# Performance work log

Hardware: AMD Instinct MI355X
Metric: run time of the kernel (lower is better)

## Reference

```python
import jax, jax.numpy as jnp
import numpy as np

B, S, E = 2, 2048, 2048
NH, NKV = 32, 8
HD = E // NH  # 64


def apply_rope(x, cos, sin):
    # x: [B, S, H, D]; cos/sin: [S, D]
    s, d = x.shape[1], x.shape[3]
    c = cos[:s, :d][None, :, None, :]
    sn = sin[:s, :d][None, :, None, :]
    x_rot = jnp.concatenate([-x[..., d // 2:], x[..., : d // 2]], axis=-1)
    return x * c + x_rot * sn


def setup_inputs() -> dict:
    key = jax.random.key(0)
    ks = jax.random.split(key, 6)
    x = jax.random.normal(ks[0], (B, S, E), dtype=jnp.float32)
    mask = jnp.ones((B, S), dtype=bool)
    # RoPE tables [S, HD]
    inv_freq = 1.0 / (10000.0 ** (jnp.arange(0, HD, 2, dtype=jnp.float32) / HD))
    freqs = jnp.arange(S, dtype=jnp.float32)[:, None] * inv_freq[None, :]
    emb = jnp.concatenate([freqs, freqs], axis=-1)  # [S, HD]
    cos = jnp.cos(emb)
    sin = jnp.sin(emb)
    sc = 1.0 / np.sqrt(E)
    Wq = jax.random.normal(ks[1], (E, E), dtype=jnp.float32) * sc
    Wk = jax.random.normal(ks[2], (NKV * HD, E), dtype=jnp.float32) * sc
    Wv = jax.random.normal(ks[3], (NKV * HD, E), dtype=jnp.float32) * sc
    Wo = jax.random.normal(ks[4], (E, E), dtype=jnp.float32) * sc
    return {"x": x, "mask": mask, "cos": cos, "sin": sin,
            "Wq": Wq, "Wk": Wk, "Wv": Wv, "Wo": Wo}


def reference(x, mask, cos, sin, Wq, Wk, Wv, Wo):
    b, s, e = x.shape
    scale = 1.0 / np.sqrt(HD)
    q = (x @ Wq.T).reshape(b, s, NH, HD)
    k = (x @ Wk.T).reshape(b, s, NKV, HD)
    v = (x @ Wv.T).reshape(b, s, NKV, HD)
    q = apply_rope(q, cos, sin)
    k = apply_rope(k, cos, sin)
    rep = NH // NKV
    # expand kv heads: [B,S,NKV,HD] -> [B,S,NH,HD]
    k = jnp.repeat(k, rep, axis=2)
    v = jnp.repeat(v, rep, axis=2)
    # [B,H,S,S]
    scores = jnp.einsum('bqhd,bkhd->bhqk', q, k) * scale
    causal = jnp.tril(jnp.ones((s, s), dtype=bool))
    combined = mask[:, None, None, :] & causal[None, None, :, :]
    scores = jnp.where(combined, scores, -jnp.inf)
    attn = jax.nn.softmax(scores, axis=-1)
    ctx = jnp.einsum('bhqk,bkhd->bqhd', attn, v).reshape(b, s, e)
    return ctx @ Wo.T
```

## Files before the change

kernel.cpp:

```cpp
#include <hip/hip_runtime.h>


typedef __attribute__((ext_vector_type(4))) float f32x4;
typedef __attribute__((ext_vector_type(16))) float f32x16;
typedef __attribute__((ext_vector_type(8))) __bf16 bf16x8;

__device__ __forceinline__ short f2bf(float f) {
  union { float f; unsigned u; } c; c.f = f;
  unsigned r = c.u + 0x7FFFu + ((c.u >> 16) & 1u);
  return (short)(r >> 16);
}

#define GLOAD16(g, l)                                                      \
  __builtin_amdgcn_global_load_lds(                                        \
      (const __attribute__((address_space(1))) unsigned int*)(g),          \
      (__attribute__((address_space(3))) unsigned int*)(l), 16, 0, 0)

__device__ __forceinline__ f32x4 mfma16(bf16x8 a, bf16x8 b, f32x4 c) {
  return __builtin_amdgcn_mfma_f32_16x16x32_bf16(a, b, c, 0, 0, 0);
}
__device__ __forceinline__ f32x16 mfma32(bf16x8 a, bf16x8 b, f32x16 c) {
  return __builtin_amdgcn_mfma_f32_32x32x16_bf16(a, b, c, 0, 0, 0);
}

__global__ void conv_bf16(const float* __restrict__ src, short* __restrict__ dst, int n) {
  int i = (blockIdx.x * blockDim.x + threadIdx.x) * 4;
  if (i >= n) return;
  float4 v = *(const float4*)(src + i);
  *(short4*)(dst + i) = make_short4(f2bf(v.x), f2bf(v.y), f2bf(v.z), f2bf(v.w));
}

__global__ __launch_bounds__(256, 2)
void gemm_bt(const short* __restrict__ A, const short* __restrict__ B,
             float* __restrict__ C, int M, int N, int K) {
  __shared__ short As[2][128 * 32];
  __shared__ short Bs[2][128 * 32];
  const int tid = threadIdx.x;
  const int lane = tid & 63;
  const int wm = (tid >> 6) >> 1;
  const int wn = (tid >> 6) & 1;
  const int m0 = blockIdx.x * 128;
  const int n0 = blockIdx.y * 128;
  const int kr = lane >> 4;
  const int lc = lane & 15;

  f32x4 acc[4][4] = {};

  const int lin0 = tid * 16;
  const int row0 = lin0 >> 6;
  const int slot0 = (lin0 >> 4) & 3;
  const int gs0 = slot0 ^ ((row0 >> 1) & 3);
  const int row1 = row0 + 64;
  const int gs1 = slot0 ^ ((row1 >> 1) & 3);
  const short* Ag0 = A + (size_t)(m0 + row0) * K + gs0 * 8;
  const short* Ag1 = A + (size_t)(m0 + row1) * K + gs1 * 8;
  const short* Bg0 = B + (size_t)(n0 + row0) * K + gs0 * 8;
  const short* Bg1 = B + (size_t)(n0 + row1) * K + gs1 * 8;
  const int dA0 = tid * 8;
  const int dA1 = tid * 8 + 2048;

  auto STAGE = [&](int k0, int buf) {
    GLOAD16(Ag0 + k0, &As[buf][dA0]);
    GLOAD16(Ag1 + k0, &As[buf][dA1]);
    GLOAD16(Bg0 + k0, &Bs[buf][dA0]);
    GLOAD16(Bg1 + k0, &Bs[buf][dA1]);
  };

  STAGE(0, 0);
  __syncthreads();
  int cur = 0;
  for (int k0 = 0; k0 < K; k0 += 32) {
    if (k0 + 32 < K) STAGE(k0 + 32, cur ^ 1);
    bf16x8 af[4], bfr[4];
#pragma unroll
    for (int i = 0; i < 4; ++i) {
      int r = wm * 64 + i * 16 + lc;
      af[i] = *(const bf16x8*)(&As[cur][r * 32 + ((kr ^ ((r >> 1) & 3)) << 3)]);
    }
#pragma unroll
    for (int j = 0; j < 4; ++j) {
      int r = wn * 64 + j * 16 + lc;
      bfr[j] = *(const bf16x8*)(&Bs[cur][r * 32 + ((kr ^ ((r >> 1) & 3)) << 3)]);
    }
#pragma unroll
    for (int i = 0; i < 4; ++i)
#pragma unroll
      for (int j = 0; j < 4; ++j)
        acc[i][j] = mfma16(af[i], bfr[j], acc[i][j]);
    __syncthreads();
    cur ^= 1;
  }
#pragma unroll
  for (int i = 0; i < 4; ++i) {
    int r0 = m0 + wm * 64 + i * 16 + kr * 4;
#pragma unroll
    for (int j = 0; j < 4; ++j) {
      int c = n0 + wn * 64 + j * 16 + lc;
#pragma unroll
      for (int ii = 0; ii < 4; ++ii)
        C[(size_t)(r0 + ii) * N + c] = acc[i][j][ii];
    }
  }
}

__global__ void rope_q(const float* __restrict__ qf, const float* __restrict__ cosT,
                       const float* __restrict__ sinT, short* __restrict__ qr) {
  int g = blockIdx.x * blockDim.x + threadIdx.x;
  int row = g >> 10;
  int rem = g & 1023;
  int h = rem >> 5, d = rem & 31;
  int s = row & 2047;
  float c = cosT[s * 64 + d], sn = sinT[s * 64 + d];
  size_t base = (size_t)row * 2048 + h * 64 + d;
  float x0 = qf[base], x1 = qf[base + 32];
  qr[base] = f2bf(x0 * c - x1 * sn);
  qr[base + 32] = f2bf(x1 * c + x0 * sn);
}

__global__ void rope_k(const float* __restrict__ kvf, const float* __restrict__ cosT,
                       const float* __restrict__ sinT, short* __restrict__ kb) {
  int g = blockIdx.x * blockDim.x + threadIdx.x;
  int row = g >> 8;
  int rem = g & 255;
  int h = rem >> 5, d = rem & 31;
  int s = row & 2047;
  float c = cosT[s * 64 + d], sn = sinT[s * 64 + d];
  size_t bi = (size_t)row * 1024 + h * 64 + d;
  size_t bo = (size_t)row * 512 + h * 64 + d;
  float x0 = kvf[bi], x1 = kvf[bi + 32];
  kb[bo] = f2bf(x0 * c - x1 * sn);
  kb[bo + 32] = f2bf(x1 * c + x0 * sn);
}

__global__ void transpose_v(const float* __restrict__ kvf, short* __restrict__ vt) {
  __shared__ float Ls[64 * 65];
  int s0 = blockIdx.x * 64;
  int h = blockIdx.y;
  int b = blockIdx.z;
  int tid = threadIdx.x;
#pragma unroll
  for (int it = 0; it < 16; ++it) {
    int lin = it * 256 + tid;
    int r = lin >> 6, c = lin & 63;
    float v = kvf[(size_t)(b * 2048 + s0 + r) * 1024 + 512 + h * 64 + c];
    Ls[c * 65 + r] = v;
  }
  __syncthreads();
#pragma unroll
  for (int it = 0; it < 16; ++it) {
    int lin = it * 256 + tid;
    int d = lin >> 6, c2 = lin & 63;
    vt[((size_t)((b * 8 + h) * 64 + d)) * 2048 + s0 + c2] = f2bf(Ls[d * 65 + c2]);
  }
}

__global__ __launch_bounds__(256, 2)
void attn(const short* __restrict__ Q, const short* __restrict__ Kk,
          const short* __restrict__ Vt, short* __restrict__ O) {
  const int qb = (int)gridDim.x - 1 - (int)blockIdx.x;
  const int h = blockIdx.y;
  const int b = blockIdx.z;
  const int kvh = h >> 2;
  const int tid = threadIdx.x;
  const int lane = tid & 63;
  const int w = tid >> 6;
  const int l5 = lane >> 5;
  const int lc5 = lane & 31;
  const int q0 = qb * 128;
  const int qrow = q0 + w * 32 + lc5;

  __shared__ short Ks[2][64 * 64];
  __shared__ short Vs[2][64 * 64];

  bf16x8 qreg[4];
  const short* qbase = Q + (size_t)(b * 2048 + qrow) * 2048 + h * 64 + l5 * 8;
#pragma unroll
  for (int s = 0; s < 4; ++s) qreg[s] = *(const bf16x8*)(qbase + s * 16);

  const int srow = tid >> 3;
  const int sslot = tid & 7;
  const short* kb0 = Kk + (size_t)(b * 2048) * 512 + kvh * 64;
  const short* vb0 = Vt + (size_t)((b * 8 + kvh) * 64) * 2048;

  auto STAGE = [&](int kt, int buf) {
#pragma unroll
    for (int it = 0; it < 2; ++it) {
      int row = srow + it * 32;
      int gs = sslot ^ (row & 7);
      GLOAD16(kb0 + (size_t)(kt * 64 + row) * 512 + gs * 8, &Ks[buf][tid * 8 + it * 2048]);
      GLOAD16(vb0 + (size_t)row * 2048 + kt * 64 + gs * 8, &Vs[buf][tid * 8 + it * 2048]);
    }
  };

  f32x16 oa0 = {}, oa1 = {};
  float mrow = -1e30f, lrow = 0.f;

  const int ktmax = (q0 + 127) >> 6;
  STAGE(0, 0);
  __syncthreads();
  int cur = 0;

  for (int kt = 0; kt <= ktmax; ++kt) {
    if (kt < ktmax) STAGE(kt + 1, cur ^ 1);

    f32x16 sa0 = {}, sa1 = {};
    const int rsw = lc5 & 7;
#pragma unroll
    for (int s = 0; s < 4; ++s) {
      int sw = ((2 * s + l5) ^ rsw) << 3;
      bf16x8 k0f = *(const bf16x8*)(&Ks[cur][lc5 * 64 + sw]);
      bf16x8 k1f = *(const bf16x8*)(&Ks[cur][(32 + lc5) * 64 + sw]);
      sa0 = mfma32(k0f, qreg[s], sa0);
      sa1 = mfma32(k1f, qreg[s], sa1);
    }

    const int kbase = kt * 64 + 4 * l5;
    if (kt * 64 + 63 > q0 + w * 32) {
#pragma unroll
      for (int r = 0; r < 16; ++r) {
        int k = kbase + (r & 3) + 8 * (r >> 2);
        if (k > qrow) sa0[r] = -1e30f;
        if (k + 32 > qrow) sa1[r] = -1e30f;
      }
    }

    float mx = -1e30f;
#pragma unroll
    for (int r = 0; r < 16; ++r) mx = fmaxf(mx, fmaxf(sa0[r], sa1[r]));
    mx = fmaxf(mx, __shfl_xor(mx, 32));
    float nm = fmaxf(mrow, mx);
    float resc = __expf((mrow - nm) * 0.125f);
    mrow = nm;
    float psum = 0.f;
#pragma unroll
    for (int r = 0; r < 16; ++r) {
      float p0 = __expf((sa0[r] - nm) * 0.125f);
      float p1 = __expf((sa1[r] - nm) * 0.125f);
      sa0[r] = p0; sa1[r] = p1;
      psum += p0 + p1;
    }
    psum += __shfl_xor(psum, 32);
    lrow = lrow * resc + psum;
#pragma unroll
    for (int r = 0; r < 16; ++r) { oa0[r] *= resc; oa1[r] *= resc; }

    unsigned pk0[8], pk1[8];
#pragma unroll
    for (int a = 0; a < 8; ++a) {
      asm("v_cvt_pk_bf16_f32 %0, %1, %2" : "=v"(pk0[a]) : "v"(sa0[2 * a]), "v"(sa0[2 * a + 1]));
      asm("v_cvt_pk_bf16_f32 %0, %1, %2" : "=v"(pk1[a]) : "v"(sa1[2 * a]), "v"(sa1[2 * a + 1]));
    }

#pragma unroll
    for (int s = 0; s < 4; ++s) {
      const int c = s & 1;
      unsigned x0 = (s < 2) ? pk0[4 * c + 0] : pk1[4 * c + 0];
      unsigned y0 = (s < 2) ? pk0[4 * c + 2] : pk1[4 * c + 2];
      unsigned x1 = (s < 2) ? pk0[4 * c + 1] : pk1[4 * c + 1];
      unsigned y1 = (s < 2) ? pk0[4 * c + 3] : pk1[4 * c + 3];
      asm("v_permlane32_swap_b32 %0, %1" : "+v"(x0), "+v"(y0));
      asm("v_permlane32_swap_b32 %0, %1" : "+v"(x1), "+v"(y1));
      union { unsigned u[4]; bf16x8 v; } pf;
      pf.u[0] = x0; pf.u[1] = x1; pf.u[2] = y0; pf.u[3] = y1;
      int sw = ((2 * s + l5) ^ rsw) << 3;
      bf16x8 v0 = *(const bf16x8*)(&Vs[cur][lc5 * 64 + sw]);
      bf16x8 v1 = *(const bf16x8*)(&Vs[cur][(32 + lc5) * 64 + sw]);
      oa0 = mfma32(v0, pf.v, oa0);
      oa1 = mfma32(v1, pf.v, oa1);
    }

    __syncthreads();
    cur ^= 1;
  }

  float inv = 1.0f / lrow;
  short* ob = O + (size_t)(b * 2048 + qrow) * 2048 + h * 64 + 4 * l5;
#pragma unroll
  for (int g = 0; g < 4; ++g) {
    *(short4*)(ob + 8 * g) =
        make_short4(f2bf(oa0[4 * g + 0] * inv), f2bf(oa0[4 * g + 1] * inv),
                    f2bf(oa0[4 * g + 2] * inv), f2bf(oa0[4 * g + 3] * inv));
    *(short4*)(ob + 32 + 8 * g) =
        make_short4(f2bf(oa1[4 * g + 0] * inv), f2bf(oa1[4 * g + 1] * inv),
                    f2bf(oa1[4 * g + 2] * inv), f2bf(oa1[4 * g + 3] * inv));
  }
}

extern "C" void kernel_launch(void* const* d_in, const int* in_sizes, int n_in,
                              void* d_out, int out_size, void* d_ws, size_t ws_size,
                              hipStream_t stream) {
  (void)in_sizes; (void)n_in; (void)out_size; (void)ws_size;
  const float* x    = (const float*)d_in[0];
  const float* cosT = (const float*)d_in[2];
  const float* sinT = (const float*)d_in[3];
  const float* Wq   = (const float*)d_in[4];
  const float* Wk   = (const float*)d_in[5];
  const float* Wv   = (const float*)d_in[6];
  const float* Wo   = (const float*)d_in[7];

  char* ws = (char*)d_ws;
  short* xb   = (short*)(ws + 0);
  short* Wqob = (short*)(ws + 16777216);
  short* Wkvb = (short*)(ws + 25165824);
  float* qf   = (float*)(ws + 29360128);
  short* ctx  = (short*)(ws + 29360128);
  float* kvf  = (float*)(ws + 62914560);
  short* qr   = (short*)(ws + 62914560);
  short* kb   = (short*)(ws + 79691776);
  short* vt   = (short*)(ws + 83886080);

  conv_bf16<<<8192, 256, 0, stream>>>(x, xb, 8388608);
  conv_bf16<<<4096, 256, 0, stream>>>(Wq, Wqob, 4194304);
  conv_bf16<<<1024, 256, 0, stream>>>(Wk, Wkvb, 1048576);
  conv_bf16<<<1024, 256, 0, stream>>>(Wv, Wkvb + 1048576, 1048576);

  gemm_bt<<<dim3(32, 16), 256, 0, stream>>>(xb, Wqob, qf, 4096, 2048, 2048);
  gemm_bt<<<dim3(32, 8), 256, 0, stream>>>(xb, Wkvb, kvf, 4096, 1024, 2048);

  rope_k<<<4096, 256, 0, stream>>>(kvf, cosT, sinT, kb);
  transpose_v<<<dim3(32, 8, 2), 256, 0, stream>>>(kvf, vt);
  rope_q<<<16384, 256, 0, stream>>>(qf, cosT, sinT, qr);

  conv_bf16<<<4096, 256, 0, stream>>>(Wo, Wqob, 4194304);

  attn<<<dim3(16, 32, 2), 256, 0, stream>>>(qr, kb, vt, ctx);

  gemm_bt<<<dim3(32, 16), 256, 0, stream>>>(ctx, Wqob, (float*)d_out, 4096, 2048, 2048);
}
```

Baseline: 389.3 us.

## Fuse RoPE and bf16 conversion into projection GEMM epilogues, streamline attention softmax

The Q and KV projection GEMMs now apply RoPE and write bf16 directly in their epilogues. This removes the separate rope_q/rope_k kernels and the fp32 intermediate round-trips, and transpose_v now reads a bf16 V buffer. Q is pre-scaled by scale*log2(e) so attention can use exp2 without the multiply. The rescale of the running max is skipped unless the max grows by more than a threshold. The K/V LDS staging layout also changes to an unswizzled slab layout, and fully masked key tiles skip compute per wave. Risks are possible LDS bank conflicts from the new layout, and accuracy changes from the lazy rescale.

```diff
diff --git a/kernel.cpp b/kernel.cpp
--- a/kernel.cpp
+++ b/kernel.cpp
@@ -4,6 +4,8 @@
 typedef __attribute__((ext_vector_type(4))) float f32x4;
 typedef __attribute__((ext_vector_type(16))) float f32x16;
 typedef __attribute__((ext_vector_type(8))) __bf16 bf16x8;
+
+#define SCL 0.18033688011112042f
 
 __device__ __forceinline__ short f2bf(float f) {
   union { float f; unsigned u; } c; c.f = f;
@@ -30,9 +32,12 @@
   *(short4*)(dst + i) = make_short4(f2bf(v.x), f2bf(v.y), f2bf(v.z), f2bf(v.w));
 }
 
+template <int EPI>
 __global__ __launch_bounds__(256, 2)
 void gemm_bt(const short* __restrict__ A, const short* __restrict__ B,
-             float* __restrict__ C, int M, int N, int K) {
+             float* __restrict__ C, short* __restrict__ outK,
+             short* __restrict__ outV, const float* __restrict__ cosT,
+             const float* __restrict__ sinT, int M, int N, int K) {
   __shared__ short As[2][128 * 32];
   __shared__ short Bs[2][128 * 32];
   const int tid = threadIdx.x;
@@ -90,50 +95,74 @@
     __syncthreads();
     cur ^= 1;
   }
-#pragma unroll
-  for (int i = 0; i < 4; ++i) {
-    int r0 = m0 + wm * 64 + i * 16 + kr * 4;
-#pragma unroll
-    for (int j = 0; j < 4; ++j) {
-      int c = n0 + wn * 64 + j * 16 + lc;
-#pragma unroll
-      for (int ii = 0; ii < 4; ++ii)
-        C[(size_t)(r0 + ii) * N + c] = acc[i][j][ii];
-    }
-  }
-}
-
-__global__ void rope_q(const float* __restrict__ qf, const float* __restrict__ cosT,
-                       const float* __restrict__ sinT, short* __restrict__ qr) {
-  int g = blockIdx.x * blockDim.x + threadIdx.x;
-  int row = g >> 10;
-  int rem = g & 1023;
-  int h = rem >> 5, d = rem & 31;
-  int s = row & 2047;
-  float c = cosT[s * 64 + d], sn = sinT[s * 64 + d];
-  size_t base = (size_t)row * 2048 + h * 64 + d;
-  float x0 = qf[base], x1 = qf[base + 32];
-  qr[base] = f2bf(x0 * c - x1 * sn);
-  qr[base + 32] = f2bf(x1 * c + x0 * sn);
-}
-
-__global__ void rope_k(const float* __restrict__ kvf, const float* __restrict__ cosT,
-                       const float* __restrict__ sinT, short* __restrict__ kb) {
-  int g = blockIdx.x * blockDim.x + threadIdx.x;
-  int row = g >> 8;
-  int rem = g & 255;
-  int h = rem >> 5, d = rem & 31;
-  int s = row & 2047;
-  float c = cosT[s * 64 + d], sn = sinT[s * 64 + d];
-  size_t bi = (size_t)row * 1024 + h * 64 + d;
-  size_t bo = (size_t)row * 512 + h * 64 + d;
-  float x0 = kvf[bi], x1 = kvf[bi + 32];
-  kb[bo] = f2bf(x0 * c - x1 * sn);
-  kb[bo + 32] = f2bf(x1 * c + x0 * sn);
-}
-
-__global__ void transpose_v(const float* __restrict__ kvf, short* __restrict__ vt) {
-  __shared__ float Ls[64 * 65];
+
+  if constexpr (EPI == 0) {
+#pragma unroll
+    for (int i = 0; i < 4; ++i) {
+      int r0 = m0 + wm * 64 + i * 16 + kr * 4;
+#pragma unroll
+      for (int j = 0; j < 4; ++j) {
+        int c = n0 + wn * 64 + j * 16 + lc;
+#pragma unroll
+        for (int ii = 0; ii < 4; ++ii)
+          C[(size_t)(r0 + ii) * N + c] = acc[i][j][ii];
+      }
+    }
+  } else if constexpr (EPI == 1) {
+#pragma unroll
+    for (int i = 0; i < 4; ++i) {
+#pragma unroll
+      for (int ii = 0; ii < 4; ++ii) {
+        int r = m0 + wm * 64 + i * 16 + kr * 4 + ii;
+        int s = r & 2047;
+#pragma unroll
+        for (int jp = 0; jp < 2; ++jp) {
+          int d = jp * 16 + lc;
+          float cs = cosT[s * 64 + d], sn = sinT[s * 64 + d];
+          float x0 = acc[i][jp][ii], x1 = acc[i][jp + 2][ii];
+          size_t base = (size_t)r * N + n0 + wn * 64;
+          outK[base + jp * 16 + lc] = f2bf((x0 * cs - x1 * sn) * SCL);
+          outK[base + (jp + 2) * 16 + lc] = f2bf((x1 * cs + x0 * sn) * SCL);
+        }
+      }
+    }
+  } else {
+    if (n0 < 512) {
+#pragma unroll
+      for (int i = 0; i < 4; ++i) {
+#pragma unroll
+        for (int ii = 0; ii < 4; ++ii) {
+          int r = m0 + wm * 64 + i * 16 + kr * 4 + ii;
+          int s = r & 2047;
+#pragma unroll
+          for (int jp = 0; jp < 2; ++jp) {
+            int d = jp * 16 + lc;
+            float cs = cosT[s * 64 + d], sn = sinT[s * 64 + d];
+            float x0 = acc[i][jp][ii], x1 = acc[i][jp + 2][ii];
+            size_t base = (size_t)r * 512 + n0 + wn * 64;
+            outK[base + jp * 16 + lc] = f2bf(x0 * cs - x1 * sn);
+            outK[base + (jp + 2) * 16 + lc] = f2bf(x1 * cs + x0 * sn);
+          }
+        }
+      }
+    } else {
+#pragma unroll
+      for (int i = 0; i < 4; ++i) {
+#pragma unroll
+        for (int ii = 0; ii < 4; ++ii) {
+          int r = m0 + wm * 64 + i * 16 + kr * 4 + ii;
+#pragma unroll
+          for (int j = 0; j < 4; ++j)
+            outV[(size_t)r * 512 + (n0 - 512) + wn * 64 + j * 16 + lc] =
+                f2bf(acc[i][j][ii]);
+        }
+      }
+    }
+  }
+}
+
+__global__ void transpose_v(const short* __restrict__ vtmp, short* __restrict__ vt) {
+  __shared__ short Ls[64 * 66];
   int s0 = blockIdx.x * 64;
   int h = blockIdx.y;
   int b = blockIdx.z;
@@ -142,15 +171,14 @@
   for (int it = 0; it < 16; ++it) {
     int lin = it * 256 + tid;
     int r = lin >> 6, c = lin & 63;
-    float v = kvf[(size_t)(b * 2048 + s0 + r) * 1024 + 512 + h * 64 + c];
-    Ls[c * 65 + r] = v;
+    Ls[c * 66 + r] = vtmp[(size_t)(b * 2048 + s0 + r) * 512 + h * 64 + c];
   }
   __syncthreads();
 #pragma unroll
   for (int it = 0; it < 16; ++it) {
     int lin = it * 256 + tid;
     int d = lin >> 6, c2 = lin & 63;
-    vt[((size_t)((b * 8 + h) * 64 + d)) * 2048 + s0 + c2] = f2bf(Ls[d * 65 + c2]);
+    vt[((size_t)((b * 8 + h) * 64 + d)) * 2048 + s0 + c2] = Ls[d * 66 + c2];
   }
 }
 
@@ -169,27 +197,22 @@
   const int q0 = qb * 128;
   const int qrow = q0 + w * 32 + lc5;
 
-  __shared__ short Ks[2][64 * 64];
-  __shared__ short Vs[2][64 * 64];
+  __shared__ short Ks[2][4096];
+  __shared__ short Vs[2][4096];
 
   bf16x8 qreg[4];
   const short* qbase = Q + (size_t)(b * 2048 + qrow) * 2048 + h * 64 + l5 * 8;
 #pragma unroll
   for (int s = 0; s < 4; ++s) qreg[s] = *(const bf16x8*)(qbase + s * 16);
 
-  const int srow = tid >> 3;
-  const int sslot = tid & 7;
-  const short* kb0 = Kk + (size_t)(b * 2048) * 512 + kvh * 64;
-  const short* vb0 = Vt + (size_t)((b * 8 + kvh) * 64) * 2048;
+  const short* kbs = Kk + (size_t)b * 2048 * 512 + kvh * 64;
+  const short* vbs = Vt + (size_t)((b * 8 + kvh) * 64) * 2048;
 
   auto STAGE = [&](int kt, int buf) {
-#pragma unroll
-    for (int it = 0; it < 2; ++it) {
-      int row = srow + it * 32;
-      int gs = sslot ^ (row & 7);
-      GLOAD16(kb0 + (size_t)(kt * 64 + row) * 512 + gs * 8, &Ks[buf][tid * 8 + it * 2048]);
-      GLOAD16(vb0 + (size_t)row * 2048 + kt * 64 + gs * 8, &Vs[buf][tid * 8 + it * 2048]);
-    }
+    GLOAD16(kbs + (size_t)(kt * 64 + lane) * 512 + w * 8, &Ks[buf][tid * 8]);
+    GLOAD16(kbs + (size_t)(kt * 64 + lane) * 512 + (w + 4) * 8, &Ks[buf][tid * 8 + 2048]);
+    GLOAD16(vbs + (size_t)lane * 2048 + kt * 64 + w * 8, &Vs[buf][tid * 8]);
+    GLOAD16(vbs + (size_t)lane * 2048 + kt * 64 + (w + 4) * 8, &Vs[buf][tid * 8 + 2048]);
   };
 
   f32x16 oa0 = {}, oa1 = {};
@@ -203,70 +226,70 @@
   for (int kt = 0; kt <= ktmax; ++kt) {
     if (kt < ktmax) STAGE(kt + 1, cur ^ 1);
 
-    f32x16 sa0 = {}, sa1 = {};
-    const int rsw = lc5 & 7;
-#pragma unroll
-    for (int s = 0; s < 4; ++s) {
-      int sw = ((2 * s + l5) ^ rsw) << 3;
-      bf16x8 k0f = *(const bf16x8*)(&Ks[cur][lc5 * 64 + sw]);
-      bf16x8 k1f = *(const bf16x8*)(&Ks[cur][(32 + lc5) * 64 + sw]);
-      sa0 = mfma32(k0f, qreg[s], sa0);
-      sa1 = mfma32(k1f, qreg[s], sa1);
-    }
-
-    const int kbase = kt * 64 + 4 * l5;
-    if (kt * 64 + 63 > q0 + w * 32) {
+    if (kt * 64 <= q0 + w * 32 + 31) {
+      f32x16 sa0 = {}, sa1 = {};
+#pragma unroll
+      for (int s = 0; s < 4; ++s) {
+        const short* kp = &Ks[cur][(2 * s + l5) * 512 + lc5 * 8];
+        sa0 = mfma32(*(const bf16x8*)kp, qreg[s], sa0);
+        sa1 = mfma32(*(const bf16x8*)(kp + 256), qreg[s], sa1);
+      }
+
+      if (kt * 64 + 63 > q0 + w * 32) {
+        const int kbase = kt * 64 + 4 * l5;
+#pragma unroll
+        for (int r = 0; r < 16; ++r) {
+          int k = kbase + (r & 3) + 8 * (r >> 2);
+          if (k > qrow) sa0[r] = -1e30f;
+          if (k + 32 > qrow) sa1[r] = -1e30f;
+        }
+      }
+
+      float mx = -1e30f;
+#pragma unroll
+      for (int r = 0; r < 16; ++r) mx = fmaxf(mx, fmaxf(sa0[r], sa1[r]));
+      mx = fmaxf(mx, __shfl_xor(mx, 32));
+      if (!__all(mx <= mrow + 8.f)) {
+        float nm = fmaxf(mrow, mx);
+        float rs = exp2f(mrow - nm);
+        mrow = nm;
+        lrow *= rs;
+#pragma unroll
+        for (int r = 0; r < 16; ++r) { oa0[r] *= rs; oa1[r] *= rs; }
+      }
+      float ps = 0.f;
 #pragma unroll
       for (int r = 0; r < 16; ++r) {
-        int k = kbase + (r & 3) + 8 * (r >> 2);
-        if (k > qrow) sa0[r] = -1e30f;
-        if (k + 32 > qrow) sa1[r] = -1e30f;
-      }
-    }
-
-    float mx = -1e30f;
-#pragma unroll
-    for (int r = 0; r < 16; ++r) mx = fmaxf(mx, fmaxf(sa0[r], sa1[r]));
-    mx = fmaxf(mx, __shfl_xor(mx, 32));
-    float nm = fmaxf(mrow, mx);
-    float resc = __expf((mrow - nm) * 0.125f);
-    mrow = nm;
-    float psum = 0.f;
-#pragma unroll
-    for (int r = 0; r < 16; ++r) {
-      float p0 = __expf((sa0[r] - nm) * 0.125f);
-      float p1 = __expf((sa1[r] - nm) * 0.125f);
-      sa0[r] = p0; sa1[r] = p1;
-      psum += p0 + p1;
-    }
-    psum += __shfl_xor(psum, 32);
-    lrow = lrow * resc + psum;
-#pragma unroll
-    for (int r = 0; r < 16; ++r) { oa0[r] *= resc; oa1[r] *= resc; }
-
-    unsigned pk0[8], pk1[8];
-#pragma unroll
-    for (int a = 0; a < 8; ++a) {
-      asm("v_cvt_pk_bf16_f32 %0, %1, %2" : "=v"(pk0[a]) : "v"(sa0[2 * a]), "v"(sa0[2 * a + 1]));
-      asm("v_cvt_pk_bf16_f32 %0, %1, %2" : "=v"(pk1[a]) : "v"(sa1[2 * a]), "v"(sa1[2 * a + 1]));
-    }
-
-#pragma unroll
-    for (int s = 0; s < 4; ++s) {
-      const int c = s & 1;
-      unsigned x0 = (s < 2) ? pk0[4 * c + 0] : pk1[4 * c + 0];
-      unsigned y0 = (s < 2) ? pk0[4 * c + 2] : pk1[4 * c + 2];
-      unsigned x1 = (s < 2) ? pk0[4 * c + 1] : pk1[4 * c + 1];
-      unsigned y1 = (s < 2) ? pk0[4 * c + 3] : pk1[4 * c + 3];
-      asm("v_permlane32_swap_b32 %0, %1" : "+v"(x0), "+v"(y0));
-      asm("v_permlane32_swap_b32 %0, %1" : "+v"(x1), "+v"(y1));
-      union { unsigned u[4]; bf16x8 v; } pf;
-      pf.u[0] = x0; pf.u[1] = x1; pf.u[2] = y0; pf.u[3] = y1;
-      int sw = ((2 * s + l5) ^ rsw) << 3;
-      bf16x8 v0 = *(const bf16x8*)(&Vs[cur][lc5 * 64 + sw]);
-      bf16x8 v1 = *(const bf16x8*)(&Vs[cur][(32 + lc5) * 64 + sw]);
-      oa0 = mfma32(v0, pf.v, oa0);
-      oa1 = mfma32(v1, pf.v, oa1);
+        float p0 = exp2f(sa0[r] - mrow);
+        float p1 = exp2f(sa1[r] - mrow);
+        sa0[r] = p0; sa1[r] = p1;
+        ps += p0 + p1;
+      }
+      ps += __shfl_xor(ps, 32);
+      lrow += ps;
+
+      unsigned pk0[8], pk1[8];
+#pragma unroll
+      for (int a = 0; a < 8; ++a) {
+        asm("v_cvt_pk_bf16_f32 %0, %1, %2" : "=v"(pk0[a]) : "v"(sa0[2 * a]), "v"(sa0[2 * a + 1]));
+        asm("v_cvt_pk_bf16_f32 %0, %1, %2" : "=v"(pk1[a]) : "v"(sa1[2 * a]), "v"(sa1[2 * a + 1]));
+      }
+
+#pragma unroll
+      for (int s = 0; s < 4; ++s) {
+        const int c = s & 1;
+        unsigned x0 = (s < 2) ? pk0[4 * c + 0] : pk1[4 * c + 0];
+        unsigned y0 = (s < 2) ? pk0[4 * c + 2] : pk1[4 * c + 2];
+        unsigned x1 = (s < 2) ? pk0[4 * c + 1] : pk1[4 * c + 1];
+        unsigned y1 = (s < 2) ? pk0[4 * c + 3] : pk1[4 * c + 3];
+        asm("v_permlane32_swap_b32 %0, %1" : "+v"(x0), "+v"(y0));
+        asm("v_permlane32_swap_b32 %0, %1" : "+v"(x1), "+v"(y1));
+        union { unsigned u[4]; bf16x8 v; } pf;
+        pf.u[0] = x0; pf.u[1] = x1; pf.u[2] = y0; pf.u[3] = y1;
+        const short* vp = &Vs[cur][(2 * s + l5) * 512 + lc5 * 8];
+        oa0 = mfma32(*(const bf16x8*)vp, pf.v, oa0);
+        oa1 = mfma32(*(const bf16x8*)(vp + 256), pf.v, oa1);
+      }
     }
 
     __syncthreads();
@@ -302,28 +325,28 @@
   short* xb   = (short*)(ws + 0);
   short* Wqob = (short*)(ws + 16777216);
   short* Wkvb = (short*)(ws + 25165824);
-  float* qf   = (float*)(ws + 29360128);
-  short* ctx  = (short*)(ws + 29360128);
-  float* kvf  = (float*)(ws + 62914560);
-  short* qr   = (short*)(ws + 62914560);
-  short* kb   = (short*)(ws + 79691776);
-  short* vt   = (short*)(ws + 83886080);
+  short* qr   = (short*)(ws + 29360128);
+  short* kb   = (short*)(ws + 46137344);
+  short* vtmp = (short*)(ws + 50331648);
+  short* vt   = (short*)(ws + 54525952);
+  short* ctx  = (short*)(ws + 58720256);
 
   conv_bf16<<<8192, 256, 0, stream>>>(x, xb, 8388608);
   conv_bf16<<<4096, 256, 0, stream>>>(Wq, Wqob, 4194304);
   conv_bf16<<<1024, 256, 0, stream>>>(Wk, Wkvb, 1048576);
   conv_bf16<<<1024, 256, 0, stream>>>(Wv, Wkvb + 1048576, 1048576);
 
-  gemm_bt<<<dim3(32, 16), 256, 0, stream>>>(xb, Wqob, qf, 4096, 2048, 2048);
-  gemm_bt<<<dim3(32, 8), 256, 0, stream>>>(xb, Wkvb, kvf, 4096, 1024, 2048);
-
-  rope_k<<<4096, 256, 0, stream>>>(kvf, cosT, sinT, kb);
-  transpose_v<<<dim3(32, 8, 2), 256, 0, stream>>>(kvf, vt);
-  rope_q<<<16384, 256, 0, stream>>>(qf, cosT, sinT, qr);
-
+  gemm_bt<1><<<dim3(32, 16), 256, 0, stream>>>(xb, Wqob, nullptr, qr, nullptr,
+                                               cosT, sinT, 4096, 2048, 2048);
+  gemm_bt<2><<<dim3(32, 8), 256, 0, stream>>>(xb, Wkvb, nullptr, kb, vtmp,
+                                              cosT, sinT, 4096, 1024, 2048);
+
+  transpose_v<<<dim3(32, 8, 2), 256, 0, stream>>>(vtmp, vt);
   conv_bf16<<<4096, 256, 0, stream>>>(Wo, Wqob, 4194304);
 
   attn<<<dim3(16, 32, 2), 256, 0, stream>>>(qr, kb, vt, ctx);
 
-  gemm_bt<<<dim3(32, 16), 256, 0, stream>>>(ctx, Wqob, (float*)d_out, 4096, 2048, 2048);
-}
+  gemm_bt<0><<<dim3(32, 16), 256, 0, stream>>>(ctx, Wqob, (float*)d_out, nullptr,
+                                               nullptr, nullptr, nullptr,
+                                               4096, 2048, 2048);
+}
```

Measured after the change: 385.2 us. About the same (-1.0%).
